# Optimization experiments

Hardware: AMD Instinct MI355X
Metric: run time of the kernel (lower is better)

The kernel has to match this reference:

```python
import jax, jax.numpy as jnp
import numpy as np

N = 100000
E = 1600000
IN_CH = 128
OUT_CH = 128
NUM_REL = 16
NUM_BASES = 8


def setup_inputs() -> dict:
    key = jax.random.key(0)
    k1, k2, k3, k4, k5, k6 = jax.random.split(key, 6)
    x = jax.random.normal(k1, (N, IN_CH), dtype=jnp.float32)
    edge_index = jax.random.randint(k2, (2, E), 0, N, dtype=jnp.int64)
    edge_type = jax.random.randint(k3, (E,), 0, NUM_REL, dtype=jnp.int64)
    # glorot-style init for basis weights (last slot = root weight) and comp
    wscale = np.sqrt(6.0 / (IN_CH + OUT_CH)).astype(np.float32)
    weight = jax.random.uniform(k4, (NUM_BASES + 1, IN_CH, OUT_CH), dtype=jnp.float32,
                                minval=-wscale, maxval=wscale)
    cscale = np.sqrt(6.0 / (NUM_REL + NUM_BASES)).astype(np.float32)
    comp = jax.random.uniform(k5, (NUM_REL, NUM_BASES), dtype=jnp.float32,
                              minval=-cscale, maxval=cscale)
    bias = jnp.zeros((OUT_CH,), dtype=jnp.float32)
    return {"x": x, "weight": weight, "comp": comp, "bias": bias,
            "edge_index": edge_index, "edge_type": edge_type, "num_nodes": N}


def reference(x, weight, comp, bias, edge_index, edge_type, num_nodes):
    """RGCN with basis decomposition, mean aggregation, root weight + bias.

    agg[i, b, :] = (1/deg(i)) * sum_{e: dst(e)=i} comp[etype(e), b] * x[src(e)]
    out = concat_b(agg, x_root) @ weight.reshape(-1, out_ch) + bias
    """
    src = edge_index[0]
    dst = edge_index[1]
    num_bases = comp.shape[1]
    coeff = comp[edge_type]            # [E, B] per-edge basis coefficients
    msg = x[src]                       # [E, in] gathered neighbor features
    # per-basis scatter-add into destination nodes (loop over small fixed B)
    aggs = [jax.ops.segment_sum(msg * coeff[:, b:b + 1], dst, num_segments=num_nodes)
            for b in range(num_bases)]
    agg = jnp.stack(aggs, axis=1)      # [N, B, in]
    # mean normalization by in-degree of destination node
    deg = jax.ops.segment_sum(jnp.ones((src.shape[0],), dtype=x.dtype), dst,
                              num_segments=num_nodes)
    agg = agg / jnp.maximum(deg, 1.0)[:, None, None]
    # [N, (B+1)*in]: bases first, then root features (matches weight layout)
    feat = jnp.concatenate([agg.reshape(num_nodes, -1), x], axis=1)
    out = feat @ weight.reshape(-1, weight.shape[-1]) + bias
    return out
```

## Files before the change

### kernel.cpp

```cpp
#include <hip/hip_runtime.h>
#include <hip/hip_bf16.h>
#include <stdint.h>


#define FPAD 1160
#define SCAT_CH 8192
#define PADV 16
#define BKCAP 2560
#define CSTRIDE 3584

typedef __attribute__((ext_vector_type(8))) __bf16 bf16x8;
typedef __attribute__((ext_vector_type(4))) float f32x4;
typedef __attribute__((ext_vector_type(2))) float f32x2;

#define RFL(v) __builtin_amdgcn_readfirstlane(v)

__global__ __launch_bounds__(256) void k_prep(const float* __restrict__ x,
                                              uint8_t* __restrict__ xq, int n4,
                                              const float* __restrict__ W,
                                              __hip_bfloat16* __restrict__ Wf,
                                              const float* __restrict__ comp,
                                              float* __restrict__ comp17,
                                              int xbB, int wpB) {
    int b = blockIdx.x;
    if (b < xbB) {
        int i = b * 256 + threadIdx.x;
        if (i < n4) {
            float4 v = ((const float4*)x)[i];
            uint32_t q = __builtin_amdgcn_cvt_pk_fp8_f32(v.x, v.y, 0u, 0);
            q = __builtin_amdgcn_cvt_pk_fp8_f32(v.z, v.w, q, 1);
            ((uint32_t*)xq)[i] = q;
        }
    } else if (b < xbB + wpB) {
        int idx = (b - xbB) * 256 + threadIdx.x;
        if (idx < 1152 * 128) {
            int k = idx >> 7, n = idx & 127;
            int kb = k >> 5, hi = (k >> 3) & 3, j = k & 7;
            Wf[((((kb << 2) + hi) << 7 | n) << 3) | j] = __float2bfloat16(W[idx]);
        }
    } else {
        int t = threadIdx.x;
        if (t < 136) comp17[t] = (t < 128) ? comp[t] : 0.f;
    }
}

__global__ __launch_bounds__(256) void k_bscatter(const int* __restrict__ src,
                                                  const int* __restrict__ dst,
                                                  const int* __restrict__ et,
                                                  int E, int NB,
                                                  int* __restrict__ cursor,
                                                  int* __restrict__ brec) {
    extern __shared__ int sm[];
    int* cnt = sm;
    int* gb  = sm + NB;
    for (int i = threadIdx.x; i < NB; i += 256) cnt[i] = 0;
    __syncthreads();
    int e0 = blockIdx.x * SCAT_CH;
    int e1 = min(e0 + SCAT_CH, E);
    for (int e = e0 + threadIdx.x; e < e1; e += 256)
        atomicAdd(&cnt[dst[e] >> 7], 1);
    __syncthreads();
    for (int i = threadIdx.x; i < NB; i += 256) {
        int c = cnt[i];
        gb[i] = c ? atomicAdd(&cursor[i], c) : 0;
    }
    __syncthreads();
    for (int i = threadIdx.x; i < NB; i += 256) cnt[i] = 0;
    __syncthreads();
    for (int e = e0 + threadIdx.x; e < e1; e += 256) {
        int d = dst[e];
        int bk = d >> 7;
        int off = gb[bk] + atomicAdd(&cnt[bk], 1);
        if (off < BKCAP)
            brec[bk * BKCAP + off] = (src[e] << 11) | ((d & 127) << 4) | (et[e] & 15);
    }
}

__global__ __launch_bounds__(256) void k_bsort(const int* __restrict__ brec,
                                               const int* __restrict__ cursor,
                                               int N,
                                               int* __restrict__ rps,
                                               int* __restrict__ dga,
                                               int* __restrict__ csr) {
    __shared__ int cnt[128], st[128];
    __shared__ int sptot;
    int b = blockIdx.x;
    int ne = min(cursor[b], BKCAP);
    int rbase = b * BKCAP;
    int pbase = b * CSTRIDE;
    int t = threadIdx.x;
    if (t < 128) cnt[t] = 0;
    __syncthreads();
    for (int i = t; i < ne; i += 256)
        atomicAdd(&cnt[(brec[rbase + i] >> 4) & 127], 1);
    __syncthreads();
    if (t < 128) st[t] = (cnt[t] + 7) & ~7;
    __syncthreads();
    for (int off = 1; off < 128; off <<= 1) {
        int u = 0;
        if (t < 128 && t >= off) u = st[t - off];
        __syncthreads();
        if (t < 128) st[t] += u;
        __syncthreads();
    }
    if (t < 128) {
        int pexcl = st[t] - ((cnt[t] + 7) & ~7);
        int d = b * 128 + t;
        if (d < N) { rps[d] = pbase + pexcl; dga[d] = cnt[t]; }
        cnt[t] = pexcl;
    }
    if (t == 127) sptot = st[127];
    __syncthreads();
    int fillN = min(sptot + 24, CSTRIDE);
    for (int i = t; i < fillN; i += 256) csr[pbase + i] = PADV;
    __syncthreads();
    for (int i = t; i < ne; i += 256) {
        int r = brec[rbase + i];
        int d7 = (r >> 4) & 127;
        int off = atomicAdd(&cnt[d7], 1);
        csr[pbase + off] = ((r >> 11) << 5) | (r & 15);
    }
}

#define GATH(pp) ((uint32_t)xq16[(uint32_t)((pp) >> 5) * 64u + (uint32_t)lane])

#define CONS1(pp, raw) do {                                               \
    uint32_t _r = (raw);                                                  \
    float _x0 = __builtin_amdgcn_cvt_f32_fp8(_r, 0);                      \
    float _x1 = __builtin_amdgcn_cvt_f32_fp8(_r, 1);                      \
    const f32x2* _cf = (const f32x2*)(comp17 + ((pp) & 31) * 8);          \
    f32x2 _xx0 = (f32x2){_x0, _x0};                                       \
    f32x2 _xx1 = (f32x2){_x1, _x1};                                       \
    f32x2 _c0 = _cf[0], _c1 = _cf[1], _c2 = _cf[2], _c3 = _cf[3];         \
    a0[0] += _c0 * _xx0; a0[1] += _c1 * _xx0;                             \
    a0[2] += _c2 * _xx0; a0[3] += _c3 * _xx0;                             \
    a1[0] += _c0 * _xx1; a1[1] += _c1 * _xx1;                             \
    a1[2] += _c2 * _xx1; a1[3] += _c3 * _xx1;                             \
} while (0)

__global__ __launch_bounds__(512, 8) void k_fused(const uint8_t* __restrict__ xq,
                                                  const float* __restrict__ x,
                                                  const float* __restrict__ comp17,
                                                  const int* __restrict__ rps,
                                                  const int* __restrict__ dga,
                                                  const int* __restrict__ csr,
                                                  const __hip_bfloat16* __restrict__ Wf,
                                                  const float* __restrict__ bias,
                                                  float* __restrict__ out, int M) {
    __shared__ __hip_bfloat16 fl[16][FPAD];
    __shared__ int snext;
    const uint16_t* __restrict__ xq16 = (const uint16_t*)xq;
    int t = threadIdx.x;
    int wid = t >> 6, lane = t & 63;
    int i0 = blockIdx.x * 16;
    if (t == 0) snext = 0;
    __syncthreads();

    #pragma unroll 1
    while (true) {
        int grab = 0;
        if (lane == 0) grab = atomicAdd(&snext, 1);
        int lr = RFL(__shfl(grab, 0));
        if (lr >= 16) break;
        int iu = i0 + lr;
        f32x2 a0[4], a1[4];
        #pragma unroll
        for (int b = 0; b < 4; b++) { a0[b] = (f32x2){0.f, 0.f}; a1[b] = (f32x2){0.f, 0.f}; }
        int s0 = 0, dg = 0;
        if (iu < M) {
            s0 = RFL(rps[iu]);
            dg = RFL(dga[iu]);
        }

        if (dg > 0) {
            int plen = (dg + 7) & ~7;
            int s1 = s0 + plen;
            int jj = s0;
            int p0 = RFL(csr[jj]),     p1 = RFL(csr[jj + 1]);
            int p2 = RFL(csr[jj + 2]), p3 = RFL(csr[jj + 3]);
            int p4 = RFL(csr[jj + 4]), p5 = RFL(csr[jj + 5]);
            int p6 = RFL(csr[jj + 6]), p7 = RFL(csr[jj + 7]);
            uint32_t w0 = GATH(p0), w1 = GATH(p1), w2 = GATH(p2), w3 = GATH(p3);
            uint32_t w4 = GATH(p4), w5 = GATH(p5), w6 = GATH(p6), w7 = GATH(p7);
            int q0 = RFL(csr[jj + 8]),  q1 = RFL(csr[jj + 9]);
            int q2 = RFL(csr[jj + 10]), q3 = RFL(csr[jj + 11]);
            int q4 = RFL(csr[jj + 12]), q5 = RFL(csr[jj + 13]);
            int q6 = RFL(csr[jj + 14]), q7 = RFL(csr[jj + 15]);
            uint32_t v0 = GATH(q0), v1 = GATH(q1), v2 = GATH(q2), v3 = GATH(q3);
            uint32_t v4 = GATH(q4), v5 = GATH(q5), v6 = GATH(q6), v7 = GATH(q7);

            #pragma unroll 1
            while (jj + 16 < s1) {
                int r0 = RFL(csr[jj + 16]), r1 = RFL(csr[jj + 17]);
                int r2 = RFL(csr[jj + 18]), r3 = RFL(csr[jj + 19]);
                int r4 = RFL(csr[jj + 20]), r5 = RFL(csr[jj + 21]);
                int r6 = RFL(csr[jj + 22]), r7 = RFL(csr[jj + 23]);
                uint32_t u0 = GATH(r0), u1 = GATH(r1), u2 = GATH(r2), u3 = GATH(r3);
                uint32_t u4 = GATH(r4), u5 = GATH(r5), u6 = GATH(r6), u7 = GATH(r7);
                CONS1(p0, w0); CONS1(p1, w1); CONS1(p2, w2); CONS1(p3, w3);
                CONS1(p4, w4); CONS1(p5, w5); CONS1(p6, w6); CONS1(p7, w7);
                p0 = q0; p1 = q1; p2 = q2; p3 = q3;
                p4 = q4; p5 = q5; p6 = q6; p7 = q7;
                w0 = v0; w1 = v1; w2 = v2; w3 = v3;
                w4 = v4; w5 = v5; w6 = v6; w7 = v7;
                q0 = r0; q1 = r1; q2 = r2; q3 = r3;
                q4 = r4; q5 = r5; q6 = r6; q7 = r7;
                v0 = u0; v1 = u1; v2 = u2; v3 = u3;
                v4 = u4; v5 = u5; v6 = u6; v7 = u7;
                jj += 8;
            }
            CONS1(p0, w0); CONS1(p1, w1); CONS1(p2, w2); CONS1(p3, w3);
            CONS1(p4, w4); CONS1(p5, w5); CONS1(p6, w6); CONS1(p7, w7);
            if (jj + 8 < s1) {
                CONS1(q0, v0); CONS1(q1, v1); CONS1(q2, v2); CONS1(q3, v3);
                CONS1(q4, v4); CONS1(q5, v5); CONS1(q6, v6); CONS1(q7, v7);
            }
        }

        float inv = 1.0f / fmaxf((float)dg, 1.0f);
        #pragma unroll
        for (int b = 0; b < 8; b++) {
            __hip_bfloat16 h0 = __float2bfloat16(a0[b >> 1][b & 1] * inv);
            __hip_bfloat16 h1 = __float2bfloat16(a1[b >> 1][b & 1] * inv);
            uint32_t pk = ((uint32_t)*(uint16_t*)&h1 << 16) | *(uint16_t*)&h0;
            *(uint32_t*)&fl[lr][b * 128 + lane * 2] = pk;
        }
        uint32_t rr = 0u;
        if (iu < M) {
            float2 xr = *(const float2*)(x + (size_t)iu * 128 + lane * 2);
            __hip_bfloat16 r0 = __float2bfloat16(xr.x);
            __hip_bfloat16 r1 = __float2bfloat16(xr.y);
            rr = ((uint32_t)*(uint16_t*)&r1 << 16) | *(uint16_t*)&r0;
        }
        *(uint32_t*)&fl[lr][1024 + lane * 2] = rr;
    }

    int lo = lane & 15, hi = lane >> 4;
    int wcol = wid * 16 + lo;
    const bf16x8* wv = (const bf16x8*)Wf;
    bf16x8 bA = wv[(hi << 7) + wcol];
    bf16x8 bB = wv[(((1 << 2) + hi) << 7) + wcol];
    float bs = bias[wcol];
    __syncthreads();

    f32x4 acc = (f32x4){0.f, 0.f, 0.f, 0.f};
    bf16x8 aA = *(const bf16x8*)&fl[lo][hi * 8];
    bf16x8 aB = *(const bf16x8*)&fl[lo][32 + hi * 8];
    #pragma unroll 4
    for (int kb = 0; kb < 34; kb++) {
        bf16x8 aN = *(const bf16x8*)&fl[lo][(kb + 2) * 32 + hi * 8];
        bf16x8 bN = wv[((((kb + 2) << 2) + hi) << 7) + wcol];
        acc = __builtin_amdgcn_mfma_f32_16x16x32_bf16(aA, bA, acc, 0, 0, 0);
        aA = aB; bA = bB; aB = aN; bB = bN;
    }
    acc = __builtin_amdgcn_mfma_f32_16x16x32_bf16(aA, bA, acc, 0, 0, 0);
    acc = __builtin_amdgcn_mfma_f32_16x16x32_bf16(aB, bB, acc, 0, 0, 0);

    #pragma unroll
    for (int q = 0; q < 4; q++) {
        int row = i0 + hi * 4 + q;
        if (row < M)
            out[(size_t)row * 128 + wcol] = acc[q] + bs;
    }
}

extern "C" void kernel_launch(void* const* d_in, const int* in_sizes, int n_in,
                              void* d_out, int out_size, void* d_ws, size_t ws_size,
                              hipStream_t stream) {
    const float* x      = (const float*)d_in[0];
    const float* weight = (const float*)d_in[1];
    const float* comp   = (const float*)d_in[2];
    const float* bias   = (const float*)d_in[3];
    const int*   eidx   = (const int*)d_in[4];
    const int*   etype  = (const int*)d_in[5];

    int N = in_sizes[0] / 128;
    int E = in_sizes[5];
    const int* srcA = eidx;
    const int* dstA = eidx + E;
    int NB = (N + 127) >> 7;

    uint8_t* ws = (uint8_t*)d_ws;
    size_t off = 0;
    auto take = [&](size_t bytes) -> void* {
        void* p = ws + off;
        off = (off + bytes + 255) & ~(size_t)255;
        return p;
    };
    uint8_t* xq        = (uint8_t*)take((size_t)N * 128);
    __hip_bfloat16* Wf = (__hip_bfloat16*)take((size_t)1152 * 128 * sizeof(__hip_bfloat16));
    float* comp17 = (float*)take(136 * sizeof(float));
    int* rps     = (int*)take((size_t)N * sizeof(int));
    int* dga     = (int*)take((size_t)N * sizeof(int));
    int* cursor  = (int*)take((size_t)NB * sizeof(int));
    int* brec    = (int*)take((size_t)NB * BKCAP * sizeof(int));
    int* csr     = (int*)take((size_t)NB * CSTRIDE * sizeof(int));
    (void)ws_size;

    int n4 = N * 128 / 4;
    int xbB = (n4 + 255) / 256;
    int wpB = (1152 * 128 + 255) / 256;
    int scB = (E + SCAT_CH - 1) / SCAT_CH;

    hipMemsetAsync(cursor, 0, (size_t)NB * sizeof(int), stream);
    k_prep<<<xbB + wpB + 1, 256, 0, stream>>>(x, xq, n4, weight, Wf,
                                              comp, comp17, xbB, wpB);
    k_bscatter<<<scB, 256, 2 * NB * sizeof(int), stream>>>(
        srcA, dstA, etype, E, NB, cursor, brec);
    k_bsort<<<NB, 256, 0, stream>>>(brec, cursor, N, rps, dga, csr);
    k_fused<<<(N + 15) / 16, 512, 0, stream>>>(xq, x, comp17, rps, dga, csr,
                                               Wf, bias, (float*)d_out, N);
}
```

Measured before the change: 178.3 us.

## Deepen gather prefetch to three stages and precompute bf16 root features

The edge-gather loop in the fused kernel now keeps three groups of eight neighbor gathers in flight instead of two, to hide more of the latency of random fp8 row loads. The prep kernel also writes a bf16 copy of x, so the fused kernel loads the root features at half the bytes with no conversion. The cost is more live registers in a kernel bounded at 512 threads with 8 waves, extra prep-time writes of a bf16 copy, and more workspace.

New measurement: 185.6 us. +4.1%, slower.

```diff
diff --git a/kernel.cpp b/kernel.cpp
--- a/kernel.cpp
+++ b/kernel.cpp
@@ -16,7 +16,8 @@
 #define RFL(v) __builtin_amdgcn_readfirstlane(v)
 
 __global__ __launch_bounds__(256) void k_prep(const float* __restrict__ x,
-                                              uint8_t* __restrict__ xq, int n4,
+                                              uint8_t* __restrict__ xq,
+                                              __hip_bfloat16* __restrict__ xb, int n4,
                                               const float* __restrict__ W,
                                               __hip_bfloat16* __restrict__ Wf,
                                               const float* __restrict__ comp,
@@ -30,6 +31,11 @@
             uint32_t q = __builtin_amdgcn_cvt_pk_fp8_f32(v.x, v.y, 0u, 0);
             q = __builtin_amdgcn_cvt_pk_fp8_f32(v.z, v.w, q, 1);
             ((uint32_t*)xq)[i] = q;
+            __hip_bfloat16 h0 = __float2bfloat16(v.x), h1 = __float2bfloat16(v.y);
+            __hip_bfloat16 h2 = __float2bfloat16(v.z), h3 = __float2bfloat16(v.w);
+            uint32_t p0 = ((uint32_t)*(uint16_t*)&h1 << 16) | *(uint16_t*)&h0;
+            uint32_t p1 = ((uint32_t)*(uint16_t*)&h3 << 16) | *(uint16_t*)&h2;
+            ((uint2*)xb)[i] = make_uint2(p0, p1);
         }
     } else if (b < xbB + wpB) {
         int idx = (b - xbB) * 256 + threadIdx.x;
@@ -139,7 +145,7 @@
 } while (0)
 
 __global__ __launch_bounds__(512, 8) void k_fused(const uint8_t* __restrict__ xq,
-                                                  const float* __restrict__ x,
+                                                  const __hip_bfloat16* __restrict__ xb,
                                                   const float* __restrict__ comp17,
                                                   const int* __restrict__ rps,
                                                   const int* __restrict__ dga,
@@ -150,6 +156,7 @@
     __shared__ __hip_bfloat16 fl[16][FPAD];
     __shared__ int snext;
     const uint16_t* __restrict__ xq16 = (const uint16_t*)xq;
+    const uint32_t* __restrict__ xb32 = (const uint32_t*)xb;
     int t = threadIdx.x;
     int wid = t >> 6, lane = t & 63;
     int i0 = blockIdx.x * 16;
@@ -188,15 +195,21 @@
             int q6 = RFL(csr[jj + 14]), q7 = RFL(csr[jj + 15]);
             uint32_t v0 = GATH(q0), v1 = GATH(q1), v2 = GATH(q2), v3 = GATH(q3);
             uint32_t v4 = GATH(q4), v5 = GATH(q5), v6 = GATH(q6), v7 = GATH(q7);
+            int r0 = RFL(csr[jj + 16]), r1 = RFL(csr[jj + 17]);
+            int r2 = RFL(csr[jj + 18]), r3 = RFL(csr[jj + 19]);
+            int r4 = RFL(csr[jj + 20]), r5 = RFL(csr[jj + 21]);
+            int r6 = RFL(csr[jj + 22]), r7 = RFL(csr[jj + 23]);
+            uint32_t u0 = GATH(r0), u1 = GATH(r1), u2 = GATH(r2), u3 = GATH(r3);
+            uint32_t u4 = GATH(r4), u5 = GATH(r5), u6 = GATH(r6), u7 = GATH(r7);
 
             #pragma unroll 1
-            while (jj + 16 < s1) {
-                int r0 = RFL(csr[jj + 16]), r1 = RFL(csr[jj + 17]);
-                int r2 = RFL(csr[jj + 18]), r3 = RFL(csr[jj + 19]);
-                int r4 = RFL(csr[jj + 20]), r5 = RFL(csr[jj + 21]);
-                int r6 = RFL(csr[jj + 22]), r7 = RFL(csr[jj + 23]);
-                uint32_t u0 = GATH(r0), u1 = GATH(r1), u2 = GATH(r2), u3 = GATH(r3);
-                uint32_t u4 = GATH(r4), u5 = GATH(r5), u6 = GATH(r6), u7 = GATH(r7);
+            while (jj + 24 < s1) {
+                int e0_ = RFL(csr[jj + 24]), e1_ = RFL(csr[jj + 25]);
+                int e2_ = RFL(csr[jj + 26]), e3_ = RFL(csr[jj + 27]);
+                int e4_ = RFL(csr[jj + 28]), e5_ = RFL(csr[jj + 29]);
+                int e6_ = RFL(csr[jj + 30]), e7_ = RFL(csr[jj + 31]);
+                uint32_t y0 = GATH(e0_), y1 = GATH(e1_), y2 = GATH(e2_), y3 = GATH(e3_);
+                uint32_t y4 = GATH(e4_), y5 = GATH(e5_), y6 = GATH(e6_), y7 = GATH(e7_);
                 CONS1(p0, w0); CONS1(p1, w1); CONS1(p2, w2); CONS1(p3, w3);
                 CONS1(p4, w4); CONS1(p5, w5); CONS1(p6, w6); CONS1(p7, w7);
                 p0 = q0; p1 = q1; p2 = q2; p3 = q3;
@@ -207,6 +220,10 @@
                 q4 = r4; q5 = r5; q6 = r6; q7 = r7;
                 v0 = u0; v1 = u1; v2 = u2; v3 = u3;
                 v4 = u4; v5 = u5; v6 = u6; v7 = u7;
+                r0 = e0_; r1 = e1_; r2 = e2_; r3 = e3_;
+                r4 = e4_; r5 = e5_; r6 = e6_; r7 = e7_;
+                u0 = y0; u1 = y1; u2 = y2; u3 = y3;
+                u4 = y4; u5 = y5; u6 = y6; u7 = y7;
                 jj += 8;
             }
             CONS1(p0, w0); CONS1(p1, w1); CONS1(p2, w2); CONS1(p3, w3);
@@ -214,6 +231,10 @@
             if (jj + 8 < s1) {
                 CONS1(q0, v0); CONS1(q1, v1); CONS1(q2, v2); CONS1(q3, v3);
                 CONS1(q4, v4); CONS1(q5, v5); CONS1(q6, v6); CONS1(q7, v7);
+                if (jj + 16 < s1) {
+                    CONS1(r0, u0); CONS1(r1, u1); CONS1(r2, u2); CONS1(r3, u3);
+                    CONS1(r4, u4); CONS1(r5, u5); CONS1(r6, u6); CONS1(r7, u7);
+                }
             }
         }
 
@@ -225,13 +246,7 @@
             uint32_t pk = ((uint32_t)*(uint16_t*)&h1 << 16) | *(uint16_t*)&h0;
             *(uint32_t*)&fl[lr][b * 128 + lane * 2] = pk;
         }
-        uint32_t rr = 0u;
-        if (iu < M) {
-            float2 xr = *(const float2*)(x + (size_t)iu * 128 + lane * 2);
-            __hip_bfloat16 r0 = __float2bfloat16(xr.x);
-            __hip_bfloat16 r1 = __float2bfloat16(xr.y);
-            rr = ((uint32_t)*(uint16_t*)&r1 << 16) | *(uint16_t*)&r0;
-        }
+        uint32_t rr = (iu < M) ? xb32[(uint32_t)iu * 64u + lane] : 0u;
         *(uint32_t*)&fl[lr][1024 + lane * 2] = rr;
     }
 
@@ -288,6 +303,7 @@
         return p;
     };
     uint8_t* xq        = (uint8_t*)take((size_t)N * 128);
+    __hip_bfloat16* xb = (__hip_bfloat16*)take((size_t)N * 128 * sizeof(__hip_bfloat16));
     __hip_bfloat16* Wf = (__hip_bfloat16*)take((size_t)1152 * 128 * sizeof(__hip_bfloat16));
     float* comp17 = (float*)take(136 * sizeof(float));
     int* rps     = (int*)take((size_t)N * sizeof(int));
@@ -303,11 +319,11 @@
     int scB = (E + SCAT_CH - 1) / SCAT_CH;
 
     hipMemsetAsync(cursor, 0, (size_t)NB * sizeof(int), stream);
-    k_prep<<<xbB + wpB + 1, 256, 0, stream>>>(x, xq, n4, weight, Wf,
+    k_prep<<<xbB + wpB + 1, 256, 0, stream>>>(x, xq, xb, n4, weight, Wf,
                                               comp, comp17, xbB, wpB);
     k_bscatter<<<scB, 256, 2 * NB * sizeof(int), stream>>>(
         srcA, dstA, etype, E, NB, cursor, brec);
     k_bsort<<<NB, 256, 0, stream>>>(brec, cursor, N, rps, dga, csr);
-    k_fused<<<(N + 15) / 16, 512, 0, stream>>>(xq, x, comp17, rps, dga, csr,
+    k_fused<<<(N + 15) / 16, 512, 0, stream>>>(xq, xb, comp17, rps, dga, csr,
                                                Wf, bias, (float*)d_out, N);
 }
```
